# Performance work log

Hardware: AMD Instinct MI355X
Metric: run time of the kernel (lower is better)

## Reference

```python
import jax, jax.numpy as jnp
import numpy as np

B, N, EG = 128, 512, 8192          # graphs, nodes per graph, edges per graph
IN_CH, HID, K, OUT_CH = 128, 64, 32, 128
E = B * EG
NT = B * N
EPS = 1e-15


def _mincut_pool(x, adj, s_logits):
    # PyG dense_mincut_pool (mask is all-True here)
    s = jax.nn.softmax(s_logits, axis=-1)                      # [B, n, k]
    out = jnp.einsum('bnk,bnf->bkf', s, x)                     # s^T x
    out_adj = jnp.einsum('bnk,bnm,bml->bkl', s, adj, s)        # s^T A s
    mincut_num = jnp.trace(out_adj, axis1=-2, axis2=-1)
    d_flat = adj.sum(-1)                                       # node degrees
    mincut_den = jnp.einsum('bnk,bn->b', s * s, d_flat)        # tr(s^T D s)
    mincut_loss = jnp.mean(-(mincut_num / mincut_den))
    ss = jnp.einsum('bnk,bnl->bkl', s, s)
    k = s.shape[-1]
    ss_fro = jnp.sqrt(jnp.sum(ss * ss, axis=(-2, -1), keepdims=True))
    i_s = jnp.eye(k, dtype=s.dtype) / jnp.sqrt(jnp.asarray(k, s.dtype))
    ortho_loss = jnp.mean(jnp.sqrt(jnp.sum((ss / ss_fro - i_s) ** 2, axis=(-2, -1))))
    ind = jnp.arange(k)
    out_adj = out_adj.at[:, ind, ind].set(0.0)                 # zero diagonal
    d = jnp.sqrt(out_adj.sum(-1))[:, None, :] + EPS            # [B,1,k]
    out_adj = out_adj / d / jnp.swapaxes(d, 1, 2)              # sym renorm
    return out, out_adj, mincut_loss, ortho_loss, s


def _dgc(x, adj, Wr, br, Ws):
    # DenseGraphConv(aggr='add'): lin_rel(adj @ x) + lin_root(x)
    return jnp.einsum('bnm,bmf->bnf', adj, x) @ Wr + br + x @ Ws


def setup_inputs() -> dict:
    key = jax.random.key(0)
    ks = jax.random.split(key, 12)
    pos = jax.random.normal(ks[0], (NT, IN_CH), jnp.float32)
    # random within-graph edges, then offset to global node ids
    ei = jax.random.randint(ks[1], (2, B, EG), 0, N)
    off = (jnp.arange(B) * N)[None, :, None]
    edge_index = (ei + off).reshape(2, E)
    edge_attr = jax.random.uniform(ks[2], (E,), jnp.float32)   # positive weights
    batch = jnp.repeat(jnp.arange(B), N)

    def lin(k, fi, fo):
        lim = 1.0 / np.sqrt(fi)
        return jax.random.uniform(k, (fi, fo), jnp.float32, -lim, lim)

    return dict(
        pos=pos, edge_index=edge_index, edge_attr=edge_attr, batch=batch,
        W1=lin(ks[3], IN_CH, HID), b1=jnp.zeros((HID,), jnp.float32),
        Wp1=lin(ks[4], HID, 2 * K), bp1=jnp.zeros((2 * K,), jnp.float32),
        W2r=lin(ks[5], HID, HID), b2=jnp.zeros((HID,), jnp.float32),
        W2s=lin(ks[6], HID, HID),
        Wp2=lin(ks[7], HID, K), bp2=jnp.zeros((K,), jnp.float32),
        W3r=lin(ks[8], HID, OUT_CH), b3=jnp.zeros((OUT_CH,), jnp.float32),
        W3s=lin(ks[9], HID, OUT_CH),
    )


def reference(pos, edge_index, edge_attr, batch, W1, b1, Wp1, bp1,
              W2r, b2, W2s, Wp2, bp2, W3r, b3, W3s):
    row, col = edge_index[0], edge_index[1]
    # --- GCNConv(in->hid) with self-loops and symmetric normalization ---
    loop = jnp.arange(NT)
    row_sl = jnp.concatenate([row, loop])
    col_sl = jnp.concatenate([col, loop])
    ew = jnp.concatenate([edge_attr, jnp.ones((NT,), edge_attr.dtype)])
    deg = jax.ops.segment_sum(ew, col_sl, num_segments=NT)
    dis = jnp.where(deg > 0, jax.lax.rsqrt(jnp.maximum(deg, 1e-12)), 0.0)
    norm = dis[row_sl] * ew * dis[col_sl]
    xw = pos @ W1
    h = jax.ops.segment_sum(norm[:, None] * xw[row_sl], col_sl, num_segments=NT) + b1
    h = jax.nn.relu(h)
    # --- to_dense_batch (equal graph sizes -> reshape, mask all True) ---
    x = h.reshape(B, N, HID)
    # --- to_dense_adj (scatter 1s, duplicates accumulate) ---
    be = batch[row]
    adj = jnp.zeros((B, N, N), h.dtype).at[be, row - be * N, col - be * N].add(1.0)
    # --- pool 1 ---
    s1 = x @ Wp1 + bp1
    x, adj, mc1, o1, s1s = _mincut_pool(x, adj, s1)
    # --- conv2 + pool 2 ---
    x = jax.nn.relu(_dgc(x, adj, W2r, b2, W2s))
    s2 = x @ Wp2 + bp2
    x, adj, mc2, o2, s2s = _mincut_pool(x, adj, s2)
    # --- conv3 ---
    x = _dgc(x, adj, W3r, b3, W3s)
    x = x[:, None]                                             # [B, 1, K, OUT]
    agg = jnp.einsum('bnk,bkl->bnl', s1s, s2s)[:, None]        # [B, 1, N, K]
    return x, mc1 + mc2, o1 + o2, agg, adj
```

## Files before the change

### kernel.cpp

```cpp
#include <hip/hip_runtime.h>
#include <hip/hip_bf16.h>


typedef __hip_bfloat16 bf16;
#define DEV static __device__ __forceinline__
DEV float b2f(bf16 x){ return __bfloat162float(x); }
DEV bf16  f2b(float x){ return __float2bfloat16(x); }

constexpr int B_  = 128;
constexpr int N_  = 512;
constexpr int EG_ = 8192;
constexpr int E_  = B_*EG_;
constexpr int NT_ = B_*N_;

constexpr size_t OFF_MC  = (size_t)B_*32*128;
constexpr size_t OFF_O   = OFF_MC + 1;
constexpr size_t OFF_AGG = OFF_O + 1;
constexpr size_t OFF_ADJ = OFF_AGG + (size_t)B_*N_*32;

constexpr size_t PHALF = (size_t)B_*4096;

__global__ void q_init(float* den, float* losses){
  int i = threadIdx.x;
  if (i < B_) den[i] = 0.f;
  if (i < 2)  losses[i] = 0.f;
}
__global__ void q_sent(float* out, float v){
  if (threadIdx.x == 0) out[0] = v;
}

__global__ __launch_bounds__(256) void q_deg(const int* __restrict__ ei,
    const float* __restrict__ ea, float* __restrict__ dis, float* __restrict__ drow){
  __shared__ float degL[N_];
  __shared__ float drL[N_];
  int t = threadIdx.x, b = blockIdx.x, base = b*N_;
  for (int j=t; j<N_; j+=256){ degL[j] = 1.0f; drL[j] = 0.f; }
  __syncthreads();
  int e0 = b*EG_;
  for (int j=t; j<EG_; j+=256){
    int e = e0 + j;
    int r = ei[e], c = ei[E_+e];
    atomicAdd(&degL[c-base], ea[e]);
    atomicAdd(&drL [r-base], 1.0f);
  }
  __syncthreads();
  for (int j=t; j<N_; j+=256){
    dis [base+j] = rsqrtf(degL[j]);
    drow[base+j] = drL[j];
  }
}

__global__ __launch_bounds__(256) void q_csr(const int* __restrict__ ei,
    const float* __restrict__ ea, const float* __restrict__ dis,
    int* __restrict__ offC, int* __restrict__ offR,
    int* __restrict__ csrR, float* __restrict__ csrW, int* __restrict__ csrC){
  __shared__ int cC[N_], cR[N_];
  int t = threadIdx.x, b = blockIdx.x, base = b*N_, e0 = b*EG_;
  for (int j=t; j<N_; j+=256){ cC[j]=0; cR[j]=0; }
  __syncthreads();
  for (int j=t; j<EG_; j+=256){
    int e = e0 + j;
    atomicAdd(&cC[ei[E_+e]-base], 1);
    atomicAdd(&cR[ei[e]   -base], 1);
  }
  __syncthreads();
  if (t == 0){
    int aC = 0, aR = 0;
    for (int n=0; n<N_; ++n){
      int vc = cC[n], vr = cR[n];
      cC[n] = aC; cR[n] = aR;
      aC += vc; aR += vr;
    }
  }
  __syncthreads();
  for (int j=t; j<N_; j+=256){ offC[base+j] = e0 + cC[j]; offR[base+j] = e0 + cR[j]; }
  __syncthreads();
  for (int j=t; j<EG_; j+=256){
    int e = e0 + j;
    int r = ei[e], c = ei[E_+e];
    float w = dis[r]*ea[e]*dis[c];
    int p  = atomicAdd(&cC[c-base], 1);
    csrR[e0+p] = r;  csrW[e0+p] = w;
    int p2 = atomicAdd(&cR[r-base], 1);
    csrC[e0+p2] = c;
  }
}

__global__ __launch_bounds__(256) void q_xw(const float* __restrict__ pos,
    const float* __restrict__ W1, bf16* __restrict__ xw){
  __shared__ float pL[64][129];
  __shared__ float wT[128][64];
  int t = threadIdx.x;
  int n0 = blockIdx.x*64;
  for (int j=t; j<2048; j+=256){
    int n = j >> 5, c4 = j & 31;
    float4 v = *reinterpret_cast<const float4*>(pos + (size_t)(n0+n)*128 + c4*4);
    pL[n][c4*4+0]=v.x; pL[n][c4*4+1]=v.y; pL[n][c4*4+2]=v.z; pL[n][c4*4+3]=v.w;
  }
  for (int j=t; j<8192; j+=256) ((float*)wT)[j] = W1[j];
  __syncthreads();
  int ti = t>>4, tj = t&15;
  float acc[4][4];
  #pragma unroll
  for (int i=0;i<4;i++)
    #pragma unroll
    for (int j=0;j<4;j++) acc[i][j] = 0.f;
  for (int k=0; k<128; ++k){
    float xs[4], ws[4];
    #pragma unroll
    for (int i=0;i<4;i++) xs[i] = pL[ti*4+i][k];
    #pragma unroll
    for (int j=0;j<4;j++) ws[j] = wT[k][tj*4+j];
    #pragma unroll
    for (int i=0;i<4;i++)
      #pragma unroll
      for (int j=0;j<4;j++) acc[i][j] += xs[i]*ws[j];
  }
  #pragma unroll
  for (int i=0;i<4;i++)
    #pragma unroll
    for (int j=0;j<4;j++)
      xw[(size_t)(n0+ti*4+i)*64 + tj*4+j] = f2b(acc[i][j]);
}

__global__ __launch_bounds__(256) void q_gcn(const int* __restrict__ offC,
    const int* __restrict__ csrR, const float* __restrict__ csrW,
    const float* __restrict__ dis, const bf16* __restrict__ xw,
    const float* __restrict__ b1, bf16* __restrict__ x1){
  int n = (blockIdx.x*256 + threadIdx.x) >> 6;
  int f = threadIdx.x & 63;
  float d = dis[n];
  float h = d*d*b2f(xw[(size_t)n*64 + f]);
  int s = offC[n];
  int e = ((n & 511) == 511) ? ((n >> 9) + 1)*EG_ : offC[n+1];
  int j = s;
  for (; j + 3 < e; j += 4){
    int r0 = csrR[j],   r1 = csrR[j+1], r2 = csrR[j+2], r3 = csrR[j+3];
    float w0 = csrW[j], w1 = csrW[j+1], w2 = csrW[j+2], w3 = csrW[j+3];
    float v0 = b2f(xw[(size_t)r0*64 + f]);
    float v1 = b2f(xw[(size_t)r1*64 + f]);
    float v2 = b2f(xw[(size_t)r2*64 + f]);
    float v3 = b2f(xw[(size_t)r3*64 + f]);
    h += w0*v0 + w1*v1 + w2*v2 + w3*v3;
  }
  for (; j < e; ++j) h += csrW[j] * b2f(xw[(size_t)csrR[j]*64 + f]);
  h += b1[f];
  x1[(size_t)n*64 + f] = f2b(h > 0.f ? h : 0.f);
}

__global__ __launch_bounds__(256) void q_s1(const bf16* __restrict__ x1,
    const float* __restrict__ Wp1, const float* __restrict__ bp1,
    const float* __restrict__ drow, bf16* __restrict__ s1, float* __restrict__ den){
  __shared__ float xT[64][65];
  __shared__ float wT[64][64];
  __shared__ float denL;
  int t = threadIdx.x;
  int n0 = blockIdx.x*64;
  if (t == 0) denL = 0.f;
  for (int j=t; j<4096; j+=256){
    wT[j>>6][j&63] = Wp1[j];
    xT[j>>6][j&63] = b2f(x1[(size_t)n0*64 + j]);
  }
  __syncthreads();
  int ti = t>>4, tj = t&15;
  float acc[4][4];
  #pragma unroll
  for (int i=0;i<4;i++)
    #pragma unroll
    for (int j=0;j<4;j++) acc[i][j] = 0.f;
  for (int f=0; f<64; ++f){
    float xs[4], ws[4];
    #pragma unroll
    for (int i=0;i<4;i++) xs[i] = xT[ti*4+i][f];
    #pragma unroll
    for (int j=0;j<4;j++) ws[j] = wT[f][tj*4+j];
    #pragma unroll
    for (int i=0;i<4;i++)
      #pragma unroll
      for (int j=0;j<4;j++) acc[i][j] += xs[i]*ws[j];
  }
  {
    float bp[4];
    #pragma unroll
    for (int j=0;j<4;j++) bp[j] = bp1[tj*4+j];
    #pragma unroll
    for (int i=0;i<4;i++)
      #pragma unroll
      for (int j=0;j<4;j++) acc[i][j] += bp[j];
  }
  #pragma unroll
  for (int i=0;i<4;i++){
    float m = fmaxf(fmaxf(acc[i][0],acc[i][1]), fmaxf(acc[i][2],acc[i][3]));
    #pragma unroll
    for (int o=8;o>=1;o>>=1) m = fmaxf(m, __shfl_xor(m, o));
    float e[4]; float ssum = 0.f;
    #pragma unroll
    for (int j=0;j<4;j++){ e[j] = expf(acc[i][j]-m); ssum += e[j]; }
    #pragma unroll
    for (int o=8;o>=1;o>>=1) ssum += __shfl_xor(ssum, o);
    float inv = 1.f/ssum, q = 0.f;
    int n = n0 + ti*4 + i;
    #pragma unroll
    for (int j=0;j<4;j++){
      float sv = e[j]*inv;
      s1[(size_t)n*64 + tj*4 + j] = f2b(sv);
      q += sv*sv;
    }
    #pragma unroll
    for (int o=8;o>=1;o>>=1) q += __shfl_xor(q, o);
    if (tj == 0) atomicAdd(&denL, q * drow[n]);
  }
  __syncthreads();
  if (t == 0) atomicAdd(&den[n0 >> 9], denL);
}

__global__ __launch_bounds__(256) void q_u(const int* __restrict__ offR,
    const int* __restrict__ csrC, const bf16* __restrict__ s1,
    bf16* __restrict__ U){
  int n = (blockIdx.x*256 + threadIdx.x) >> 6;
  int l = threadIdx.x & 63;
  float u = 0.f;
  int s = offR[n];
  int e = ((n & 511) == 511) ? ((n >> 9) + 1)*EG_ : offR[n+1];
  int j = s;
  for (; j + 3 < e; j += 4){
    int c0 = csrC[j], c1 = csrC[j+1], c2 = csrC[j+2], c3 = csrC[j+3];
    float v0 = b2f(s1[(size_t)c0*64 + l]);
    float v1 = b2f(s1[(size_t)c1*64 + l]);
    float v2 = b2f(s1[(size_t)c2*64 + l]);
    float v3 = b2f(s1[(size_t)c3*64 + l]);
    u += v0 + v1 + v2 + v3;
  }
  for (; j < e; ++j) u += b2f(s1[(size_t)csrC[j]*64 + l]);
  U[(size_t)n*64 + l] = f2b(u);
}

__global__ __launch_bounds__(256) void q_p3(const bf16* __restrict__ s1,
    const bf16* __restrict__ U, const bf16* __restrict__ x1,
    float* __restrict__ adjPp, float* __restrict__ ssPp, float* __restrict__ X1pp){
  __shared__ float sL[64][64];
  __shared__ float uL[64][64];
  __shared__ float xL[64][64];
  int t = threadIdx.x, blk = blockIdx.x;
  int b = blk >> 1, half = blk & 1;
  int base = b*N_ + half*256;
  int ti = t>>4, tj = t&15;
  float accA[4][4], accS[4][4], accX[4][4];
  #pragma unroll
  for (int i=0;i<4;i++)
    #pragma unroll
    for (int j=0;j<4;j++){ accA[i][j]=0.f; accS[i][j]=0.f; accX[i][j]=0.f; }
  for (int c=0; c<4; ++c){
    __syncthreads();
    for (int j=t; j<4096; j+=256){
      int n = j>>6, q = j&63;
      size_t g = (size_t)(base + c*64 + n)*64 + q;
      sL[n][q] = b2f(s1[g]);
      uL[n][q] = b2f(U [g]);
      xL[n][q] = b2f(x1[g]);
    }
    __syncthreads();
    for (int n=0; n<64; ++n){
      float4 skv = *reinterpret_cast<const float4*>(&sL[n][ti*4]);
      float4 ulv = *reinterpret_cast<const float4*>(&uL[n][tj*4]);
      float4 xlv = *reinterpret_cast<const float4*>(&xL[n][tj*4]);
      float4 slv = *reinterpret_cast<const float4*>(&sL[n][tj*4]);
      float sk[4] = {skv.x, skv.y, skv.z, skv.w};
      float ul[4] = {ulv.x, ulv.y, ulv.z, ulv.w};
      float xl[4] = {xlv.x, xlv.y, xlv.z, xlv.w};
      float sl[4] = {slv.x, slv.y, slv.z, slv.w};
      #pragma unroll
      for (int i=0;i<4;i++)
        #pragma unroll
        for (int j=0;j<4;j++){
          accA[i][j] += sk[i]*ul[j];
          accS[i][j] += sk[i]*sl[j];
          accX[i][j] += sk[i]*xl[j];
        }
    }
  }
  size_t pb = (size_t)half*PHALF + (size_t)b*4096;
  #pragma unroll
  for (int i=0;i<4;i++)
    #pragma unroll
    for (int j=0;j<4;j++){
      size_t o = pb + (ti*4+i)*64 + tj*4+j;
      adjPp[o] = accA[i][j];
      ssPp [o] = accS[i][j];
      X1pp [o] = accX[i][j];
    }
}

__global__ __launch_bounds__(256) void q_norm1(const float* __restrict__ adjPp,
    const float* __restrict__ ssPp, const float* __restrict__ X1pp,
    const float* __restrict__ den, float* __restrict__ A2,
    float* __restrict__ X1n, float* __restrict__ losses){
  __shared__ float aL[4096];
  __shared__ float sL[4096];
  __shared__ float rL[64];
  __shared__ float red[4];
  int b = blockIdx.x, t = threadIdx.x;
  size_t pb = (size_t)b*4096;
  for (int j = t; j < 4096; j += 256){
    aL[j] = adjPp[pb + j] + adjPp[PHALF + pb + j];
    sL[j] = ssPp [pb + j] + ssPp [PHALF + pb + j];
    X1n[pb + j] = X1pp[pb + j] + X1pp[PHALF + pb + j];
  }
  __syncthreads();
  if (t == 0){
    float tr = 0.f;
    for (int k = 0; k < 64; ++k) tr += aL[k*64 + k];
    atomicAdd(&losses[0], -(tr/den[b]) * (1.0f/B_));
  }
  if (t < 64){
    float rs = 0.f;
    for (int l = 0; l < 64; ++l) rs += aL[t*64 + l];
    rs -= aL[t*64 + t];
    rL[t] = 1.f/(sqrtf(rs) + 1e-15f);
  }
  float pp = 0.f;
  for (int j = t; j < 4096; j += 256){ float v = sL[j]; pp += v*v; }
  #pragma unroll
  for (int o = 32; o >= 1; o >>= 1) pp += __shfl_xor(pp, o);
  if ((t & 63) == 0) red[t >> 6] = pp;
  __syncthreads();
  float fro = sqrtf(red[0]+red[1]+red[2]+red[3]);
  __syncthreads();
  float op = 0.f;
  for (int j = t; j < 4096; j += 256){
    int kk = j >> 6, ll = j & 63;
    float v = sL[j]/fro - ((kk==ll) ? 0.125f : 0.f);
    op += v*v;
  }
  #pragma unroll
  for (int o = 32; o >= 1; o >>= 1) op += __shfl_xor(op, o);
  if ((t & 63) == 0) red[t >> 6] = op;
  __syncthreads();
  if (t == 0) atomicAdd(&losses[1], sqrtf(red[0]+red[1]+red[2]+red[3]) * (1.0f/B_));
  for (int j = t; j < 4096; j += 256){
    int kk = j >> 6, ll = j & 63;
    A2[(size_t)b*4096 + j] = (kk==ll) ? 0.f : aL[j]*rL[kk]*rL[ll];
  }
}

__global__ __launch_bounds__(256) void q_lvl2(const float* __restrict__ X1p,
    const float* __restrict__ A2g,
    const float* __restrict__ W2r, const float* __restrict__ b2,
    const float* __restrict__ W2s, const float* __restrict__ Wp2,
    const float* __restrict__ bp2, const float* __restrict__ W3r,
    const float* __restrict__ b3, const float* __restrict__ W3s,
    float* __restrict__ s2f, float* __restrict__ out, float* __restrict__ losses){
  __shared__ float XL[64][64], AL[64][64], AXL[64][64], x2L[64][64];
  __shared__ float s2L[64][32], VL[64][32];
  __shared__ float adj2L[32][32], ss2L[32][32], A3L[32][32];
  __shared__ float o2L[32][64], GL[32][64];
  __shared__ float wp2L[64][32];
  __shared__ float r2L[32], red[4];
  __shared__ float den2s;
  int t = threadIdx.x, b = blockIdx.x;
  int wv = t>>6, lane = t&63;
  for (int j=t; j<4096; j+=256){
    ((float*)XL)[j] = X1p[(size_t)b*4096 + j];
    ((float*)AL)[j] = A2g[(size_t)b*4096 + j];
  }
  for (int j=t; j<2048; j+=256) ((float*)wp2L)[j] = Wp2[j];
  __syncthreads();
  for (int i=0;i<16;i++){
    int n = wv*16+i; float a = 0.f;
    for (int m=0;m<64;m++) a += AL[n][m]*XL[m][lane];
    AXL[n][lane] = a;
  }
  __syncthreads();
  {
    float bb = b2[lane];
    for (int i=0;i<16;i++){
      int n = wv*16+i; float a = bb;
      for (int m=0;m<64;m++) a += AXL[n][m]*W2r[m*64+lane];
      for (int m=0;m<64;m++) a += XL[n][m]*W2s[m*64+lane];
      x2L[n][lane] = a > 0.f ? a : 0.f;
    }
  }
  __syncthreads();
  {
    int k = lane & 31;
    for (int i=0;i<16;i++){
      int n = wv*16+i;
      float lgv = bp2[k];
      for (int f=0; f<64; f++) lgv += x2L[n][f]*wp2L[f][k];
      float m = lgv;
      #pragma unroll
      for (int o=16;o>=1;o>>=1) m = fmaxf(m, __shfl_xor(m, o));
      float p = expf(lgv - m), ssum = p;
      #pragma unroll
      for (int o=16;o>=1;o>>=1) ssum += __shfl_xor(ssum, o);
      float sv = p/ssum;
      s2L[n][k] = sv;
      s2f[(size_t)b*2048 + n*32 + k] = sv;
    }
  }
  __syncthreads();
  {
    float part = 0.f;
    if (t < 64){
      float rs = 0.f; for (int m=0;m<64;m++) rs += AL[t][m];
      float q  = 0.f; for (int k2=0;k2<32;k2++){ float s = s2L[t][k2]; q += s*s; }
      part = q*rs;
    }
    #pragma unroll
    for (int o=32;o>=1;o>>=1) part += __shfl_xor(part, o);
    if (t == 0) den2s = part;
  }
  __syncthreads();
  for (int j=0;j<8;j++){
    int idx = t + 256*j; int n = idx>>5, l = idx&31;
    float a = 0.f;
    for (int m=0;m<64;m++) a += AL[n][m]*s2L[m][l];
    VL[n][l] = a;
  }
  __syncthreads();
  for (int j=0;j<4;j++){
    int idx = t + 256*j; int k2 = idx>>5, l = idx&31;
    float a = 0.f, c2 = 0.f;
    for (int n=0;n<64;n++){ float s = s2L[n][k2]; a += s*VL[n][l]; c2 += s*s2L[n][l]; }
    adj2L[k2][l] = a; ss2L[k2][l] = c2;
  }
  __syncthreads();
  if (t == 0){
    float tr = 0.f; for (int k2=0;k2<32;k2++) tr += adj2L[k2][k2];
    atomicAdd(&losses[0], -(tr/den2s) * (1.0f/B_));
  }
  if (t < 32){
    float rs = 0.f; for (int l=0;l<32;l++) rs += adj2L[t][l];
    rs -= adj2L[t][t];
    r2L[t] = 1.f/(sqrtf(rs) + 1e-15f);
  }
  {
    float pp = 0.f;
    for (int j=t; j<1024; j+=256){ float v = ((float*)ss2L)[j]; pp += v*v; }
    #pragma unroll
    for (int o=32;o>=1;o>>=1) pp += __shfl_xor(pp, o);
    if ((t & 63) == 0) red[t >> 6] = pp;
    __syncthreads();
    float fro = sqrtf(red[0]+red[1]+red[2]+red[3]);
    __syncthreads();
    float op = 0.f;
    for (int j=t; j<1024; j+=256){
      int k2 = j>>5, l = j&31;
      float v = ((float*)ss2L)[j]/fro - ((k2==l) ? 0.1767766952966369f : 0.f);
      op += v*v;
    }
    #pragma unroll
    for (int o=32;o>=1;o>>=1) op += __shfl_xor(op, o);
    if ((t & 63) == 0) red[t >> 6] = op;
    __syncthreads();
    if (t == 0) atomicAdd(&losses[1], sqrtf(red[0]+red[1]+red[2]+red[3]) * (1.0f/B_));
  }
  __syncthreads();
  for (int j=0;j<4;j++){
    int idx = t + 256*j; int k2 = idx>>5, l = idx&31;
    float v = (k2==l) ? 0.f : adj2L[k2][l]*r2L[k2]*r2L[l];
    A3L[k2][l] = v;
    out[OFF_ADJ + (size_t)b*1024 + idx] = v;
  }
  __syncthreads();
  for (int j=0;j<8;j++){
    int idx = t + 256*j; int k2 = idx>>6, f = idx&63;
    float a = 0.f;
    for (int n=0;n<64;n++) a += s2L[n][k2]*x2L[n][f];
    o2L[k2][f] = a;
  }
  __syncthreads();
  for (int j=0;j<8;j++){
    int idx = t + 256*j; int n = idx>>6, f = idx&63;
    float a = 0.f;
    for (int m=0;m<32;m++) a += A3L[n][m]*o2L[m][f];
    GL[n][f] = a;
  }
  __syncthreads();
  for (int j=0;j<16;j++){
    int idx = t + 256*j; int n = idx>>7, o = idx&127;
    float a = b3[o];
    for (int f=0;f<64;f++) a += GL[n][f]*W3r[f*128+o];
    for (int f=0;f<64;f++) a += o2L[n][f]*W3s[f*128+o];
    out[(size_t)b*4096 + idx] = a;
  }
}

__global__ __launch_bounds__(256) void q_agg(const bf16* __restrict__ s1,
    const float* __restrict__ s2, float* __restrict__ out){
  __shared__ float s1L[64][65];
  __shared__ float s2L[64][33];
  int t = threadIdx.x, blk = blockIdx.x;
  int b = blk >> 3, n0 = (blk & 7)*64;
  for (int j=t; j<4096; j+=256){
    int n = j>>6, k = j&63;
    s1L[n][k] = b2f(s1[((size_t)b*N_ + n0 + n)*64 + k]);
  }
  for (int j=t; j<2048; j+=256){
    int k = j>>5, l = j&31;
    s2L[k][l] = s2[(size_t)b*2048 + j];
  }
  __syncthreads();
  int ti = t>>4, tj = t&15;
  float acc[4][2];
  #pragma unroll
  for (int i=0;i<4;i++){ acc[i][0]=0.f; acc[i][1]=0.f; }
  for (int k=0; k<64; ++k){
    float xs[4];
    #pragma unroll
    for (int i=0;i<4;i++) xs[i] = s1L[ti*4+i][k];
    float w0 = s2L[k][tj*2], w1 = s2L[k][tj*2+1];
    #pragma unroll
    for (int i=0;i<4;i++){ acc[i][0] += xs[i]*w0; acc[i][1] += xs[i]*w1; }
  }
  #pragma unroll
  for (int i=0;i<4;i++){
    size_t o = OFF_AGG + ((size_t)b*N_ + n0 + ti*4+i)*32 + tj*2;
    out[o]   = acc[i][0];
    out[o+1] = acc[i][1];
  }
}

__global__ void q_loss(const float* losses, float* out){
  if (threadIdx.x == 0){
    out[OFF_MC] = losses[0];
    out[OFF_O]  = losses[1];
  }
}

extern "C" void kernel_launch(void* const* d_in, const int* in_sizes, int n_in,
                              void* d_out, int out_size, void* d_ws, size_t ws_size,
                              hipStream_t stream){
  (void)out_size;
  float* out = (float*)d_out;

  static const long long EXP_SIZES[16] = {
    8388608LL, 2097152LL, 1048576LL, 65536LL,
    8192LL, 64LL, 4096LL, 64LL,
    4096LL, 64LL, 4096LL, 2048LL, 32LL,
    8192LL, 128LL, 8192LL };
  if (n_in != 16){ q_sent<<<1,64,0,stream>>>(out, exp2f(36.f)); return; }
  for (int i = 0; i < 16; ++i){
    if ((long long)in_sizes[i] != EXP_SIZES[i]){
      q_sent<<<1,64,0,stream>>>(out, exp2f((float)(37+i))); return;
    }
  }

  const float* pos = (const float*)d_in[0];
  const int*   ei  = (const int*)  d_in[1];
  const float* ea  = (const float*)d_in[2];
  const float* W1  = (const float*)d_in[4];
  const float* b1  = (const float*)d_in[5];
  const float* Wp1 = (const float*)d_in[6];
  const float* bp1 = (const float*)d_in[7];
  const float* W2r = (const float*)d_in[8];
  const float* b2  = (const float*)d_in[9];
  const float* W2s = (const float*)d_in[10];
  const float* Wp2 = (const float*)d_in[11];
  const float* bp2 = (const float*)d_in[12];
  const float* W3r = (const float*)d_in[13];
  const float* b3  = (const float*)d_in[14];
  const float* W3s = (const float*)d_in[15];

  constexpr size_t MB2 = (size_t)B_*4096*4;
  char* w = (char*)d_ws;
  float* dis    = (float*)w; w += (size_t)NT_*4;
  float* drow   = (float*)w; w += (size_t)NT_*4;
  float* den    = (float*)w; w += (size_t)B_*4;
  float* losses = (float*)w; w += 64;
  int*   offC   = (int*)  w; w += (size_t)NT_*4;
  int*   offR   = (int*)  w; w += (size_t)NT_*4;
  char*  R1     = w;         w += 2*MB2;
  char*  R2     = w;         w += 2*MB2;
  char*  R3     = w;         w += 2*MB2;
  float* A2n    = (float*)w; w += MB2;
  float* X1n    = (float*)w; w += MB2;
  float* s2     = (float*)w; w += (size_t)B_*2048*4;
  bf16*  xwU    = (bf16*)w;  w += (size_t)NT_*64*2;
  bf16*  x1     = (bf16*)w;  w += (size_t)NT_*64*2;
  bf16*  s1     = (bf16*)w;  w += (size_t)NT_*64*2;
  size_t need = (size_t)(w - (char*)d_ws);
  if (ws_size < need){ q_sent<<<1,64,0,stream>>>(out, exp2f(20.f)); return; }

  int*   csrR  = (int*)  R1;
  float* csrW  = (float*)R2;
  int*   csrC  = (int*)  R3;
  float* adjPp = (float*)R1;
  float* ssPp  = (float*)R2;
  float* X1pp  = (float*)R3;

  q_init <<<1,    256, 0, stream>>>(den, losses);
  q_deg  <<<B_,   256, 0, stream>>>(ei, ea, dis, drow);
  q_csr  <<<B_,   256, 0, stream>>>(ei, ea, dis, offC, offR, csrR, csrW, csrC);
  q_xw   <<<NT_/64,256, 0, stream>>>(pos, W1, xwU);
  q_gcn  <<<16384,256, 0, stream>>>(offC, csrR, csrW, dis, xwU, b1, x1);
  q_s1   <<<NT_/64,256, 0, stream>>>(x1, Wp1, bp1, drow, s1, den);
  q_u    <<<16384,256, 0, stream>>>(offR, csrC, s1, xwU);
  q_p3   <<<B_*2, 256, 0, stream>>>(s1, xwU, x1, adjPp, ssPp, X1pp);
  q_norm1<<<B_,   256, 0, stream>>>(adjPp, ssPp, X1pp, den, A2n, X1n, losses);
  q_lvl2 <<<B_,   256, 0, stream>>>(X1n, A2n, W2r, b2, W2s, Wp2, bp2,
                                    W3r, b3, W3s, s2, out, losses);
  q_agg  <<<1024, 256, 0, stream>>>(s1, s2, out);
  q_loss <<<1,     64, 0, stream>>>(losses, out);
}
```

Baseline: 313.7 us.

## Fuse degree and CSR build kernels; register-tile level-2 matmuls with padded LDS

Merges the degree and CSR construction kernels into one per-graph kernel that computes edge weights from shared-memory degrees. This drops one launch and a second pass over the edge list. Rewrites the dense 64x64 and output-projection matmuls in the level-2 kernel as 4x4 register tiles per thread with float4 weight loads. Pads shared arrays by one column to avoid bank conflicts. The larger shared footprint and higher register use could lower occupancy, but this kernel already runs only one block per graph.

```diff
diff --git a/kernel.cpp b/kernel.cpp
--- a/kernel.cpp
+++ b/kernel.cpp
@@ -29,41 +29,29 @@
   if (threadIdx.x == 0) out[0] = v;
 }
 
-__global__ __launch_bounds__(256) void q_deg(const int* __restrict__ ei,
-    const float* __restrict__ ea, float* __restrict__ dis, float* __restrict__ drow){
+__global__ __launch_bounds__(256) void q_degcsr(const int* __restrict__ ei,
+    const float* __restrict__ ea, float* __restrict__ dis, float* __restrict__ drow,
+    int* __restrict__ offC, int* __restrict__ offR,
+    int* __restrict__ csrR, float* __restrict__ csrW, int* __restrict__ csrC){
   __shared__ float degL[N_];
   __shared__ float drL[N_];
-  int t = threadIdx.x, b = blockIdx.x, base = b*N_;
-  for (int j=t; j<N_; j+=256){ degL[j] = 1.0f; drL[j] = 0.f; }
-  __syncthreads();
-  int e0 = b*EG_;
+  __shared__ int cC[N_], cR[N_];
+  int t = threadIdx.x, b = blockIdx.x, base = b*N_, e0 = b*EG_;
+  for (int j=t; j<N_; j+=256){ degL[j]=1.0f; drL[j]=0.f; cC[j]=0; cR[j]=0; }
+  __syncthreads();
   for (int j=t; j<EG_; j+=256){
     int e = e0 + j;
     int r = ei[e], c = ei[E_+e];
     atomicAdd(&degL[c-base], ea[e]);
     atomicAdd(&drL [r-base], 1.0f);
+    atomicAdd(&cC[c-base], 1);
+    atomicAdd(&cR[r-base], 1);
   }
   __syncthreads();
   for (int j=t; j<N_; j+=256){
     dis [base+j] = rsqrtf(degL[j]);
     drow[base+j] = drL[j];
   }
-}
-
-__global__ __launch_bounds__(256) void q_csr(const int* __restrict__ ei,
-    const float* __restrict__ ea, const float* __restrict__ dis,
-    int* __restrict__ offC, int* __restrict__ offR,
-    int* __restrict__ csrR, float* __restrict__ csrW, int* __restrict__ csrC){
-  __shared__ int cC[N_], cR[N_];
-  int t = threadIdx.x, b = blockIdx.x, base = b*N_, e0 = b*EG_;
-  for (int j=t; j<N_; j+=256){ cC[j]=0; cR[j]=0; }
-  __syncthreads();
-  for (int j=t; j<EG_; j+=256){
-    int e = e0 + j;
-    atomicAdd(&cC[ei[E_+e]-base], 1);
-    atomicAdd(&cR[ei[e]   -base], 1);
-  }
-  __syncthreads();
   if (t == 0){
     int aC = 0, aR = 0;
     for (int n=0; n<N_; ++n){
@@ -78,7 +66,7 @@
   for (int j=t; j<EG_; j+=256){
     int e = e0 + j;
     int r = ei[e], c = ei[E_+e];
-    float w = dis[r]*ea[e]*dis[c];
+    float w = rsqrtf(degL[r-base])*ea[e]*rsqrtf(degL[c-base]);
     int p  = atomicAdd(&cC[c-base], 1);
     csrR[e0+p] = r;  csrW[e0+p] = w;
     int p2 = atomicAdd(&cR[r-base], 1);
@@ -350,35 +338,71 @@
     const float* __restrict__ bp2, const float* __restrict__ W3r,
     const float* __restrict__ b3, const float* __restrict__ W3s,
     float* __restrict__ s2f, float* __restrict__ out, float* __restrict__ losses){
-  __shared__ float XL[64][64], AL[64][64], AXL[64][64], x2L[64][64];
-  __shared__ float s2L[64][32], VL[64][32];
-  __shared__ float adj2L[32][32], ss2L[32][32], A3L[32][32];
-  __shared__ float o2L[32][64], GL[32][64];
-  __shared__ float wp2L[64][32];
+  __shared__ float XL[64][65], AL[64][65], AXL[64][65], x2L[64][65];
+  __shared__ float s2L[64][33], VL[64][33];
+  __shared__ float adj2L[32][33], ss2L[32][33], A3L[32][33];
+  __shared__ float o2L[32][65], GL[32][65];
+  __shared__ float wp2L[64][33];
   __shared__ float r2L[32], red[4];
   __shared__ float den2s;
   int t = threadIdx.x, b = blockIdx.x;
   int wv = t>>6, lane = t&63;
+  int ti = t>>4, tj = t&15;
   for (int j=t; j<4096; j+=256){
-    ((float*)XL)[j] = X1p[(size_t)b*4096 + j];
-    ((float*)AL)[j] = A2g[(size_t)b*4096 + j];
-  }
-  for (int j=t; j<2048; j+=256) ((float*)wp2L)[j] = Wp2[j];
-  __syncthreads();
-  for (int i=0;i<16;i++){
-    int n = wv*16+i; float a = 0.f;
-    for (int m=0;m<64;m++) a += AL[n][m]*XL[m][lane];
-    AXL[n][lane] = a;
-  }
+    int n = j>>6, q = j&63;
+    XL[n][q] = X1p[(size_t)b*4096 + j];
+    AL[n][q] = A2g[(size_t)b*4096 + j];
+  }
+  for (int j=t; j<2048; j+=256){ int f = j>>5, k = j&31; wp2L[f][k] = Wp2[j]; }
   __syncthreads();
   {
-    float bb = b2[lane];
-    for (int i=0;i<16;i++){
-      int n = wv*16+i; float a = bb;
-      for (int m=0;m<64;m++) a += AXL[n][m]*W2r[m*64+lane];
-      for (int m=0;m<64;m++) a += XL[n][m]*W2s[m*64+lane];
-      x2L[n][lane] = a > 0.f ? a : 0.f;
-    }
+    float acc[4][4];
+    #pragma unroll
+    for (int i=0;i<4;i++){ acc[i][0]=0.f; acc[i][1]=0.f; acc[i][2]=0.f; acc[i][3]=0.f; }
+    for (int m=0;m<64;++m){
+      float av[4], xv[4];
+      #pragma unroll
+      for (int i=0;i<4;i++) av[i] = AL[ti*4+i][m];
+      #pragma unroll
+      for (int j=0;j<4;j++) xv[j] = XL[m][tj*4+j];
+      #pragma unroll
+      for (int i=0;i<4;i++)
+        #pragma unroll
+        for (int j=0;j<4;j++) acc[i][j] += av[i]*xv[j];
+    }
+    #pragma unroll
+    for (int i=0;i<4;i++)
+      #pragma unroll
+      for (int j=0;j<4;j++) AXL[ti*4+i][tj*4+j] = acc[i][j];
+  }
+  __syncthreads();
+  {
+    float acc[4][4];
+    #pragma unroll
+    for (int i=0;i<4;i++){ acc[i][0]=0.f; acc[i][1]=0.f; acc[i][2]=0.f; acc[i][3]=0.f; }
+    for (int m=0;m<64;++m){
+      float a1[4], a2[4];
+      #pragma unroll
+      for (int i=0;i<4;i++){ a1[i] = AXL[ti*4+i][m]; a2[i] = XL[ti*4+i][m]; }
+      float4 wr = *reinterpret_cast<const float4*>(&W2r[m*64 + tj*4]);
+      float4 ws = *reinterpret_cast<const float4*>(&W2s[m*64 + tj*4]);
+      float wrv[4] = {wr.x, wr.y, wr.z, wr.w};
+      float wsv[4] = {ws.x, ws.y, ws.z, ws.w};
+      #pragma unroll
+      for (int i=0;i<4;i++)
+        #pragma unroll
+        for (int j=0;j<4;j++) acc[i][j] += a1[i]*wrv[j] + a2[i]*wsv[j];
+    }
+    float bp[4];
+    #pragma unroll
+    for (int j=0;j<4;j++) bp[j] = b2[tj*4+j];
+    #pragma unroll
+    for (int i=0;i<4;i++)
+      #pragma unroll
+      for (int j=0;j<4;j++){
+        float v = acc[i][j] + bp[j];
+        x2L[ti*4+i][tj*4+j] = v > 0.f ? v : 0.f;
+      }
   }
   __syncthreads();
   {
@@ -436,7 +460,7 @@
   }
   {
     float pp = 0.f;
-    for (int j=t; j<1024; j+=256){ float v = ((float*)ss2L)[j]; pp += v*v; }
+    for (int j=t; j<1024; j+=256){ int k2 = j>>5, l = j&31; float v = ss2L[k2][l]; pp += v*v; }
     #pragma unroll
     for (int o=32;o>=1;o>>=1) pp += __shfl_xor(pp, o);
     if ((t & 63) == 0) red[t >> 6] = pp;
@@ -446,7 +470,7 @@
     float op = 0.f;
     for (int j=t; j<1024; j+=256){
       int k2 = j>>5, l = j&31;
-      float v = ((float*)ss2L)[j]/fro - ((k2==l) ? 0.1767766952966369f : 0.f);
+      float v = ss2L[k2][l]/fro - ((k2==l) ? 0.1767766952966369f : 0.f);
       op += v*v;
     }
     #pragma unroll
@@ -477,12 +501,31 @@
     GL[n][f] = a;
   }
   __syncthreads();
-  for (int j=0;j<16;j++){
-    int idx = t + 256*j; int n = idx>>7, o = idx&127;
-    float a = b3[o];
-    for (int f=0;f<64;f++) a += GL[n][f]*W3r[f*128+o];
-    for (int f=0;f<64;f++) a += o2L[n][f]*W3s[f*128+o];
-    out[(size_t)b*4096 + idx] = a;
+  {
+    int ti2 = t>>5, tj2 = t&31;
+    float acc[4][4];
+    #pragma unroll
+    for (int i=0;i<4;i++){ acc[i][0]=0.f; acc[i][1]=0.f; acc[i][2]=0.f; acc[i][3]=0.f; }
+    for (int f=0; f<64; ++f){
+      float gv[4], ov[4];
+      #pragma unroll
+      for (int i=0;i<4;i++){ gv[i] = GL[ti2*4+i][f]; ov[i] = o2L[ti2*4+i][f]; }
+      float4 wr = *reinterpret_cast<const float4*>(&W3r[f*128 + tj2*4]);
+      float4 ws = *reinterpret_cast<const float4*>(&W3s[f*128 + tj2*4]);
+      float wrv[4] = {wr.x, wr.y, wr.z, wr.w};
+      float wsv[4] = {ws.x, ws.y, ws.z, ws.w};
+      #pragma unroll
+      for (int i=0;i<4;i++)
+        #pragma unroll
+        for (int j=0;j<4;j++) acc[i][j] += gv[i]*wrv[j] + ov[i]*wsv[j];
+    }
+    #pragma unroll
+    for (int i=0;i<4;i++)
+      #pragma unroll
+      for (int j=0;j<4;j++){
+        int n = ti2*4+i, o = tj2*4+j;
+        out[(size_t)b*4096 + n*128 + o] = acc[i][j] + b3[o];
+      }
   }
 }
 
@@ -589,17 +632,16 @@
   float* ssPp  = (float*)R2;
   float* X1pp  = (float*)R3;
 
-  q_init <<<1,    256, 0, stream>>>(den, losses);
-  q_deg  <<<B_,   256, 0, stream>>>(ei, ea, dis, drow);
-  q_csr  <<<B_,   256, 0, stream>>>(ei, ea, dis, offC, offR, csrR, csrW, csrC);
-  q_xw   <<<NT_/64,256, 0, stream>>>(pos, W1, xwU);
-  q_gcn  <<<16384,256, 0, stream>>>(offC, csrR, csrW, dis, xwU, b1, x1);
-  q_s1   <<<NT_/64,256, 0, stream>>>(x1, Wp1, bp1, drow, s1, den);
-  q_u    <<<16384,256, 0, stream>>>(offR, csrC, s1, xwU);
-  q_p3   <<<B_*2, 256, 0, stream>>>(s1, xwU, x1, adjPp, ssPp, X1pp);
-  q_norm1<<<B_,   256, 0, stream>>>(adjPp, ssPp, X1pp, den, A2n, X1n, losses);
-  q_lvl2 <<<B_,   256, 0, stream>>>(X1n, A2n, W2r, b2, W2s, Wp2, bp2,
-                                    W3r, b3, W3s, s2, out, losses);
-  q_agg  <<<1024, 256, 0, stream>>>(s1, s2, out);
-  q_loss <<<1,     64, 0, stream>>>(losses, out);
-}
+  q_init  <<<1,    256, 0, stream>>>(den, losses);
+  q_degcsr<<<B_,   256, 0, stream>>>(ei, ea, dis, drow, offC, offR, csrR, csrW, csrC);
+  q_xw    <<<NT_/64,256, 0, stream>>>(pos, W1, xwU);
+  q_gcn   <<<16384,256, 0, stream>>>(offC, csrR, csrW, dis, xwU, b1, x1);
+  q_s1    <<<NT_/64,256, 0, stream>>>(x1, Wp1, bp1, drow, s1, den);
+  q_u     <<<16384,256, 0, stream>>>(offR, csrC, s1, xwU);
+  q_p3    <<<B_*2, 256, 0, stream>>>(s1, xwU, x1, adjPp, ssPp, X1pp);
+  q_norm1 <<<B_,   256, 0, stream>>>(adjPp, ssPp, X1pp, den, A2n, X1n, losses);
+  q_lvl2  <<<B_,   256, 0, stream>>>(X1n, A2n, W2r, b2, W2s, Wp2, bp2,
+                                     W3r, b3, W3s, s2, out, losses);
+  q_agg   <<<1024, 256, 0, stream>>>(s1, s2, out);
+  q_loss  <<<1,     64, 0, stream>>>(losses, out);
+}
```

Measured after the change: 299.2 us. 1.05x faster.
